# Performance work log

Measured on AMD Instinct MI355X. Metric: run time of the kernel, lower is better.

## Reference

```python
import jax, jax.numpy as jnp
import numpy as np

N = 8192
H = 512
TAU = 0.8
LAM = 0.5
EPS = 1e-8


def setup_inputs() -> dict:
    key = jax.random.key(0)
    k1, k2, k3, k4, k5 = jax.random.split(key, 5)
    xavier_std = 1.414 * np.sqrt(2.0 / (H + H))  # xavier_normal_ with gain=1.414
    return {
        "z_mp": jax.random.normal(k1, (N, H), dtype=jnp.float32),
        "z_sc": jax.random.normal(k2, (N, H), dtype=jnp.float32),
        "pos": jax.random.randint(k3, (N, N), 0, 2, dtype=jnp.int32),
        "W1": (jax.random.normal(k4, (H, H), dtype=jnp.float32) * xavier_std),
        "b1": jnp.zeros((H,), dtype=jnp.float32),
        "W2": (jax.random.normal(k5, (H, H), dtype=jnp.float32) * xavier_std),
        "b2": jnp.zeros((H,), dtype=jnp.float32),
    }


def _proj(z, W1, b1, W2, b2):
    # nn.Linear applies x @ W.T + b
    h = jax.nn.elu(z @ W1.T + b1)
    return h @ W2.T + b2


def _sim(z1, z2, tau):
    # exp(cosine_similarity / tau), computed as in the original:
    # dot(z1, z2.T) / (|z1| |z2|.T) / tau
    n1 = jnp.linalg.norm(z1, axis=-1, keepdims=True)  # [N,1]
    n2 = jnp.linalg.norm(z2, axis=-1, keepdims=True)  # [N,1]
    dot = z1 @ z2.T                                   # [N,N]
    return jnp.exp(dot / (n1 * n2.T) / tau)


def reference(z_mp, z_sc, pos, W1, b1, W2, b2):
    pos_f = pos.astype(jnp.float32)
    zp_mp = _proj(z_mp, W1, b1, W2, b2)
    zp_sc = _proj(z_sc, W1, b1, W2, b2)

    m_mp2sc = _sim(zp_mp, zp_sc, TAU)   # [N,N]
    m_sc2mp = m_mp2sc.T                 # [N,N]

    # row-normalize, masked log-mean (mp -> sc)
    s_mp = m_mp2sc / (jnp.sum(m_mp2sc, axis=1, keepdims=True) + EPS)
    lori_mp = -jnp.mean(jnp.log(jnp.sum(s_mp * pos_f, axis=-1)))

    # row-normalize, masked log-mean (sc -> mp)
    s_sc = m_sc2mp / (jnp.sum(m_sc2mp, axis=1, keepdims=True) + EPS)
    lori_sc = -jnp.mean(jnp.log(jnp.sum(s_sc * pos_f, axis=-1)))

    return LAM * lori_mp + (1.0 - LAM) * lori_sc
```

## Files before the change

### kernel.cpp

```cpp
#include <hip/hip_runtime.h>
#include <stdint.h>


#define NN 8192
#define HH 512
#define TAUF 0.8f
#define EPSF 1e-8f
#define NW (NN / 32)

typedef __attribute__((ext_vector_type(4))) float f32x4;
typedef __attribute__((ext_vector_type(2))) int i32x2;
typedef __attribute__((ext_vector_type(4))) int i32x4;
typedef __attribute__((ext_vector_type(8))) int i32x8;
typedef unsigned short u16;
typedef unsigned int u32;
typedef uint8_t u8;

typedef __attribute__((address_space(1))) void GV;
typedef __attribute__((address_space(3))) void LV;

__device__ __forceinline__ void g2l16(const void* g, void* l) {
  __builtin_amdgcn_global_load_lds((const GV*)g, (LV*)l, 16, 0, 0);
}

__device__ __forceinline__ u32 f2fp8(float x) {
  u32 u = __builtin_bit_cast(u32, x);
  u32 s = (u >> 31) << 7;
  float a = fabsf(x);
  if (a >= 0.015625f) {
    u32 b = __builtin_bit_cast(u32, a);
    b += 0x7FFFFu + ((b >> 20) & 1u);
    u32 e = (b >> 23) - 127u + 7u;
    u32 m = (b >> 20) & 7u;
    return s | (e << 3) | m;
  } else {
    int m = (int)rintf(a * 512.0f);
    return s | (u32)m;
  }
}

__device__ __forceinline__ void cast8f8(const float* __restrict__ in, u8* __restrict__ out, int i) {
  f32x4 a = *(const f32x4*)(in + i);
  f32x4 b = *(const f32x4*)(in + i + 4);
  i32x2 v;
  v.x = (int)(f2fp8(a.x) | (f2fp8(a.y) << 8) | (f2fp8(a.z) << 16) | (f2fp8(a.w) << 24));
  v.y = (int)(f2fp8(b.x) | (f2fp8(b.y) << 8) | (f2fp8(b.z) << 16) | (f2fp8(b.w) << 24));
  *(i32x2*)(out + i) = v;
}

__global__ __launch_bounds__(256)
void prep_kernel(const int* __restrict__ pos, u32* __restrict__ P,
                 const float* __restrict__ z_mp, u8* __restrict__ zbA,
                 const float* __restrict__ z_sc, u8* __restrict__ zbB,
                 const float* __restrict__ W1, u8* __restrict__ W1b,
                 const float* __restrict__ W2, u8* __restrict__ W2b) {
  int b = blockIdx.x, tid = threadIdx.x;
  if (b < 8192) {
    int gid = b * 256 + tid;
    const int* src = pos + (size_t)gid * 32;
    u32 w = 0;
#pragma unroll
    for (int c = 0; c < 8; ++c) {
      i32x4 p = *(const i32x4*)(src + c * 4);
      w |= ((u32)p.x & 1u) << (c * 4);
      w |= ((u32)p.y & 1u) << (c * 4 + 1);
      w |= ((u32)p.z & 1u) << (c * 4 + 2);
      w |= ((u32)p.w & 1u) << (c * 4 + 3);
    }
    P[gid] = w;
  } else if (b < 10240) {
    cast8f8(z_mp, zbA, ((b - 8192) * 256 + tid) * 8);
  } else if (b < 12288) {
    cast8f8(z_sc, zbB, ((b - 10240) * 256 + tid) * 8);
  } else if (b < 12416) {
    cast8f8(W1, W1b, ((b - 12288) * 256 + tid) * 8);
  } else {
    cast8f8(W2, W2b, ((b - 12416) * 256 + tid) * 8);
  }
}

__global__ __launch_bounds__(256, 1)
void proj_fused(const u8* __restrict__ zbA, const u8* __restrict__ zbB,
                const u8* __restrict__ W1b, const float* __restrict__ b1,
                const u8* __restrict__ W2b, const float* __restrict__ b2,
                u8* __restrict__ znA, u8* __restrict__ znB) {
  __shared__ __align__(16) u8 Az[64 * 512];
  __shared__ __align__(16) u8 Hs[64 * 512];
  __shared__ __align__(16) u8 Ws[512 * 128];
  __shared__ float ssqL[4][64];
  __shared__ float invL[64];

  const int tid = threadIdx.x;
  const int lane = tid & 63, w = tid >> 6;
  const int lo = lane & 15, quad = lane >> 4;
  const int b = blockIdx.x;
  const bool isA = b < 128;
  const int m0 = (b & 127) * 64;
  const u8* zb = isA ? zbA : zbB;
  u8* zn = isA ? znA : znB;
  const float nscale = isA ? (1.0f / TAUF) : 1.0f;

  char* AzB = (char*)Az;
  char* HsB = (char*)Hs;
  char* WsB = (char*)Ws;

  {
    const int ls = lane >> 5;
    const int ch = lane & 31;
#pragma unroll
    for (int t = 0; t < 8; ++t) {
      int r = w * 16 + t * 2 + ls;
      int sw = (t * 2 + ls) & 7;
      const u8* src = zb + (size_t)(m0 + r) * HH + ((ch & ~7) | ((ch & 7) ^ sw)) * 16;
      g2l16(src, AzB + w * 8192 + t * 1024);
    }
  }
  const int srow = lane >> 3;
  const int schunk = ((lane & 7) ^ srow) * 16;
  auto stageW = [&](const u8* __restrict__ Wb, int kbyte) {
#pragma unroll
    for (int t = 0; t < 16; ++t)
      g2l16(Wb + (size_t)(w * 128 + t * 8 + srow) * HH + kbyte + schunk,
            WsB + w * 16384 + t * 1024);
  };
  stageW(W1b, 0);
  asm volatile("s_waitcnt vmcnt(0)" ::: "memory");
  __syncthreads();

  f32x4 acc[4][8];

#pragma unroll
  for (int mi = 0; mi < 4; ++mi)
#pragma unroll
    for (int ni = 0; ni < 8; ++ni) acc[mi][ni] = f32x4{0.f, 0.f, 0.f, 0.f};

#pragma unroll
  for (int k0 = 0; k0 < 4; ++k0) {
    i32x8 aF[4], bF[8];
#pragma unroll
    for (int mi = 0; mi < 4; ++mi) {
      int ar = mi * 16 + lo, sw = lo & 7;
      i32x4 p0 = *(const i32x4*)(AzB + ar * 512 + k0 * 128 + ((2 * quad) ^ sw) * 16);
      i32x4 p1 = *(const i32x4*)(AzB + ar * 512 + k0 * 128 + ((2 * quad + 1) ^ sw) * 16);
      aF[mi] = __builtin_shufflevector(p0, p1, 0, 1, 2, 3, 4, 5, 6, 7);
    }
#pragma unroll
    for (int ni = 0; ni < 8; ++ni) {
      int br = w * 128 + ni * 16 + lo, sw = br & 7;
      i32x4 p0 = *(const i32x4*)(WsB + br * 128 + ((2 * quad) ^ sw) * 16);
      i32x4 p1 = *(const i32x4*)(WsB + br * 128 + ((2 * quad + 1) ^ sw) * 16);
      bF[ni] = __builtin_shufflevector(p0, p1, 0, 1, 2, 3, 4, 5, 6, 7);
    }
    __syncthreads();
    if (k0 < 3) stageW(W1b, (k0 + 1) * 128);
    else        stageW(W2b, 0);
#pragma unroll
    for (int mi = 0; mi < 4; ++mi)
#pragma unroll
      for (int ni = 0; ni < 8; ++ni)
        acc[mi][ni] = __builtin_amdgcn_mfma_scale_f32_16x16x128_f8f6f4(
            aF[mi], bF[ni], acc[mi][ni], 0, 0, 0, 127, 0, 127);
    if (k0 < 3) __syncthreads();
  }

  {
    float b1v[8];
#pragma unroll
    for (int ni = 0; ni < 8; ++ni) b1v[ni] = b1[w * 128 + ni * 16 + lo];
#pragma unroll
    for (int mi = 0; mi < 4; ++mi)
#pragma unroll
      for (int r = 0; r < 4; ++r) {
        int row = mi * 16 + quad * 4 + r;
        int rsw = row & 7;
#pragma unroll
        for (int ni = 0; ni < 8; ++ni) {
          float v = acc[mi][ni][r] + b1v[ni];
          if (v < 0.f) v = __expf(v) - 1.f;
          int ch = w * 8 + ni;
          HsB[row * 512 + (((ch & 7) ^ rsw) | (ch & ~7)) * 16 + lo] = (char)(u8)f2fp8(v);
        }
      }
  }
  __syncthreads();

#pragma unroll
  for (int mi = 0; mi < 4; ++mi)
#pragma unroll
    for (int ni = 0; ni < 8; ++ni) acc[mi][ni] = f32x4{0.f, 0.f, 0.f, 0.f};

#pragma unroll
  for (int k0 = 0; k0 < 4; ++k0) {
    i32x8 aF[4], bF[8];
#pragma unroll
    for (int mi = 0; mi < 4; ++mi) {
      int ar = mi * 16 + lo, sw = lo & 7;
      i32x4 p0 = *(const i32x4*)(HsB + ar * 512 + k0 * 128 + ((2 * quad) ^ sw) * 16);
      i32x4 p1 = *(const i32x4*)(HsB + ar * 512 + k0 * 128 + ((2 * quad + 1) ^ sw) * 16);
      aF[mi] = __builtin_shufflevector(p0, p1, 0, 1, 2, 3, 4, 5, 6, 7);
    }
#pragma unroll
    for (int ni = 0; ni < 8; ++ni) {
      int br = w * 128 + ni * 16 + lo, sw = br & 7;
      i32x4 p0 = *(const i32x4*)(WsB + br * 128 + ((2 * quad) ^ sw) * 16);
      i32x4 p1 = *(const i32x4*)(WsB + br * 128 + ((2 * quad + 1) ^ sw) * 16);
      bF[ni] = __builtin_shufflevector(p0, p1, 0, 1, 2, 3, 4, 5, 6, 7);
    }
    if (k0 < 3) {
      __syncthreads();
      stageW(W2b, (k0 + 1) * 128);
    }
#pragma unroll
    for (int mi = 0; mi < 4; ++mi)
#pragma unroll
      for (int ni = 0; ni < 8; ++ni)
        acc[mi][ni] = __builtin_amdgcn_mfma_scale_f32_16x16x128_f8f6f4(
            aF[mi], bF[ni], acc[mi][ni], 0, 0, 0, 127, 0, 127);
    if (k0 < 3) __syncthreads();
  }

  float ssq[4][4] = {};
  {
    float b2v[8];
#pragma unroll
    for (int ni = 0; ni < 8; ++ni) b2v[ni] = b2[w * 128 + ni * 16 + lo];
#pragma unroll
    for (int mi = 0; mi < 4; ++mi)
#pragma unroll
      for (int ni = 0; ni < 8; ++ni)
#pragma unroll
        for (int r = 0; r < 4; ++r) {
          float v = acc[mi][ni][r] + b2v[ni];
          acc[mi][ni][r] = v;
          ssq[mi][r] += v * v;
        }
  }
#pragma unroll
  for (int d = 1; d < 16; d <<= 1)
#pragma unroll
    for (int mi = 0; mi < 4; ++mi)
#pragma unroll
      for (int r = 0; r < 4; ++r) ssq[mi][r] += __shfl_xor(ssq[mi][r], d, 64);
  if (lo == 0) {
#pragma unroll
    for (int mi = 0; mi < 4; ++mi)
#pragma unroll
      for (int r = 0; r < 4; ++r) ssqL[w][mi * 16 + quad * 4 + r] = ssq[mi][r];
  }
  __syncthreads();
  if (tid < 64)
    invL[tid] = nscale * rsqrtf(ssqL[0][tid] + ssqL[1][tid] + ssqL[2][tid] + ssqL[3][tid]);
  __syncthreads();

#pragma unroll
  for (int mi = 0; mi < 4; ++mi)
#pragma unroll
    for (int r = 0; r < 4; ++r) {
      int row = mi * 16 + quad * 4 + r;
      float inv = invL[row];
#pragma unroll
      for (int ni = 0; ni < 8; ++ni)
        AzB[row * 512 + w * 128 + ni * 16 + lo] = (char)(u8)f2fp8(acc[mi][ni][r] * inv);
    }
  __syncthreads();
  {
    int row = tid >> 2, seg = tid & 3;
#pragma unroll
    for (int i = 0; i < 8; ++i) {
      i32x4 v = *(const i32x4*)(AzB + row * 512 + seg * 128 + i * 16);
      *(i32x4*)(zn + (size_t)(m0 + row) * 512 + seg * 128 + i * 16) = v;
    }
  }
}

__global__ __launch_bounds__(256)
void sim_kernel(const u8* __restrict__ Az, const u8* __restrict__ Bz,
                const u32* __restrict__ Pbits,
                float* __restrict__ rowpart, float* __restrict__ posrowpart,
                float* __restrict__ colpart, float* __restrict__ poscolpart) {
  __shared__ __align__(16) u8 As[128 * 128];
  __shared__ __align__(16) u8 Bs[128 * 128];
  __shared__ u32 PBi[128 * 4];
  __shared__ u32 PBj[128 * 4];
  const int tid = threadIdx.x;
  const int lane = tid & 63, w = tid >> 6;
  const int lo = lane & 15, quad = lane >> 4;
  const int wy = w >> 1, wx = w & 1;

  const int bid = blockIdx.x + (int)gridDim.x * blockIdx.y;
  const int xcd = bid & 7, s = bid >> 3;
  const int by = xcd * 8 + (s >> 6);
  const int bx = s & 63;
  const int i0 = by * 128, j0 = bx * 128;

  const int il = tid >> 1, w2 = (tid & 1) * 2;
  const u32* PiSrc = Pbits + (size_t)(i0 + il) * NW + (j0 >> 5) + w2;
  const u32* PjSrc = Pbits + (size_t)(j0 + il) * NW + (i0 >> 5) + w2;
  u32 pa0 = PiSrc[0], pa1 = PiSrc[1], pb0 = PjSrc[0], pb1 = PjSrc[1];

  const int srow = lane >> 3;
  const int schunk = ((lane & 7) ^ srow) * 16;
  char* AsB = (char*)As; char* BsB = (char*)Bs;
  f32x4 acc[4][4] = {};

  for (int k0 = 0; k0 < HH; k0 += 128) {
    const u8* ga = Az + (size_t)(i0 + w * 32 + srow) * HH + k0 + schunk;
    const u8* gb = Bz + (size_t)(j0 + w * 32 + srow) * HH + k0 + schunk;
#pragma unroll
    for (int t = 0; t < 4; ++t) {
      g2l16(ga + (size_t)(t * 8) * HH, AsB + w * 4096 + t * 1024);
      g2l16(gb + (size_t)(t * 8) * HH, BsB + w * 4096 + t * 1024);
    }
    asm volatile("s_waitcnt vmcnt(0)" ::: "memory");
    __syncthreads();
    i32x8 aF[4], bF[4];
#pragma unroll
    for (int mi = 0; mi < 4; ++mi) {
      int ar = wy * 64 + mi * 16 + lo;
      int sw = ar & 7;
      i32x4 p0 = *(const i32x4*)(AsB + ar * 128 + ((2 * quad) ^ sw) * 16);
      i32x4 p1 = *(const i32x4*)(AsB + ar * 128 + ((2 * quad + 1) ^ sw) * 16);
      aF[mi] = __builtin_shufflevector(p0, p1, 0, 1, 2, 3, 4, 5, 6, 7);
    }
#pragma unroll
    for (int ni = 0; ni < 4; ++ni) {
      int br = wx * 64 + ni * 16 + lo;
      int sw = br & 7;
      i32x4 p0 = *(const i32x4*)(BsB + br * 128 + ((2 * quad) ^ sw) * 16);
      i32x4 p1 = *(const i32x4*)(BsB + br * 128 + ((2 * quad + 1) ^ sw) * 16);
      bF[ni] = __builtin_shufflevector(p0, p1, 0, 1, 2, 3, 4, 5, 6, 7);
    }
#pragma unroll
    for (int mi = 0; mi < 4; ++mi)
#pragma unroll
      for (int ni = 0; ni < 4; ++ni)
        acc[mi][ni] = __builtin_amdgcn_mfma_scale_f32_16x16x128_f8f6f4(
            aF[mi], bF[ni], acc[mi][ni], 0, 0, 0, 127, 0, 127);
    __syncthreads();
  }

  PBi[il * 4 + w2] = pa0; PBi[il * 4 + w2 + 1] = pa1;
  PBj[il * 4 + w2] = pb0; PBj[il * 4 + w2 + 1] = pb1;

#pragma unroll
  for (int mi = 0; mi < 4; ++mi)
#pragma unroll
    for (int ni = 0; ni < 4; ++ni)
#pragma unroll
      for (int r = 0; r < 4; ++r)
        acc[mi][ni][r] = __expf(acc[mi][ni][r]);

  __syncthreads();

  const int rowb = wy * 64 + quad * 4;
  const int colb = wx * 64 + lo;

#pragma unroll
  for (int mi = 0; mi < 4; ++mi) {
    int rl = rowb + mi * 16;
    float rs[4], pr[4];
#pragma unroll
    for (int r = 0; r < 4; ++r) {
      u32 W0 = PBi[(rl + r) * 4 + wx * 2];
      u32 W1 = PBi[(rl + r) * 4 + wx * 2 + 1];
      float e0 = acc[mi][0][r], e1 = acc[mi][1][r];
      float e2 = acc[mi][2][r], e3 = acc[mi][3][r];
      rs[r] = (e0 + e1) + (e2 + e3);
      pr[r] = (((W0 >> lo) & 1u) ? e0 : 0.f) + (((W0 >> (16 + lo)) & 1u) ? e1 : 0.f) +
              (((W1 >> lo) & 1u) ? e2 : 0.f) + (((W1 >> (16 + lo)) & 1u) ? e3 : 0.f);
    }
#pragma unroll
    for (int d = 1; d < 16; d <<= 1) {
#pragma unroll
      for (int r = 0; r < 4; ++r) {
        rs[r] += __shfl_xor(rs[r], d, 64);
        pr[r] += __shfl_xor(pr[r], d, 64);
      }
    }
    if (lo == 0) {
      float* rp = rowpart + (size_t)(bx * 2 + wx) * NN;
      float* pp = posrowpart + (size_t)(bx * 2 + wx) * NN;
#pragma unroll
      for (int r = 0; r < 4; ++r) {
        rp[i0 + rl + r] = rs[r];
        pp[i0 + rl + r] = pr[r];
      }
    }
  }

#pragma unroll
  for (int ni = 0; ni < 4; ++ni) {
    int cl = colb + ni * 16;
    u32 W0 = PBj[cl * 4 + wy * 2];
    u32 W1 = PBj[cl * 4 + wy * 2 + 1];
    float cs = 0.f, pc = 0.f;
#pragma unroll
    for (int mi = 0; mi < 4; ++mi) {
      u32 W = (mi < 2) ? W0 : W1;
      int sh = (mi & 1) * 16 + quad * 4;
#pragma unroll
      for (int r = 0; r < 4; ++r) {
        float e = acc[mi][ni][r];
        cs += e;
        pc += ((W >> (sh + r)) & 1u) ? e : 0.f;
      }
    }
    cs += __shfl_xor(cs, 16, 64); cs += __shfl_xor(cs, 32, 64);
    pc += __shfl_xor(pc, 16, 64); pc += __shfl_xor(pc, 32, 64);
    if (quad == 0) {
      colpart[(size_t)(by * 2 + wy) * NN + j0 + cl] = cs;
      poscolpart[(size_t)(by * 2 + wy) * NN + j0 + cl] = pc;
    }
  }
}

__global__ __launch_bounds__(256)
void reduce1_kernel(const float* __restrict__ rowpart, const float* __restrict__ posrowpart,
                    const float* __restrict__ colpart, const float* __restrict__ poscolpart,
                    float* __restrict__ red) {
  int t = threadIdx.x;
  int i = blockIdx.x * 128 + (t >> 1);
  int half = t & 1;
  float rs = 0.f, pr = 0.f, cs = 0.f, pc = 0.f;
  for (int s = half * 64; s < half * 64 + 64; ++s) {
    rs += rowpart[(size_t)s * NN + i];
    pr += posrowpart[(size_t)s * NN + i];
    cs += colpart[(size_t)s * NN + i];
    pc += poscolpart[(size_t)s * NN + i];
  }
  rs += __shfl_xor(rs, 1, 64); pr += __shfl_xor(pr, 1, 64);
  cs += __shfl_xor(cs, 1, 64); pc += __shfl_xor(pc, 1, 64);
  float term = (half == 0) ? (__logf(pr / (rs + EPSF)) + __logf(pc / (cs + EPSF))) : 0.f;
#pragma unroll
  for (int d = 2; d < 64; d <<= 1) term += __shfl_xor(term, d, 64);
  __shared__ float rsh[4];
  if ((t & 63) == 0) rsh[t >> 6] = term;
  __syncthreads();
  if (t == 0) red[blockIdx.x] = rsh[0] + rsh[1] + rsh[2] + rsh[3];
}

__global__ void reduce2_kernel(const float* __restrict__ red, float* __restrict__ out) {
  float s = red[threadIdx.x];
#pragma unroll
  for (int d = 1; d < 64; d <<= 1) s += __shfl_xor(s, d, 64);
  if (threadIdx.x == 0) out[0] = -0.5f * s / (float)NN;
}

extern "C" void kernel_launch(void* const* d_in, const int* in_sizes, int n_in,
                              void* d_out, int out_size, void* d_ws, size_t ws_size,
                              hipStream_t stream) {
  const float* z_mp = (const float*)d_in[0];
  const float* z_sc = (const float*)d_in[1];
  const int* pos = (const int*)d_in[2];
  const float* W1 = (const float*)d_in[3];
  const float* b1 = (const float*)d_in[4];
  const float* W2 = (const float*)d_in[5];
  const float* b2 = (const float*)d_in[6];
  float* out = (float*)d_out;

  char* ws = (char*)d_ws;
  u32* Pbits = (u32*)(ws);
  u8* zbA = (u8*)(ws + 8388608);
  u8* zbB = (u8*)(ws + 16777216);
  u8* W1b = (u8*)(ws + 25165824);
  u8* W2b = (u8*)(ws + 25690112);
  float* rowpart    = (float*)(ws + 26214400);
  float* posrowpart = (float*)(ws + 30408704);
  float* colpart    = (float*)(ws + 34603008);
  float* poscolpart = (float*)(ws + 38797312);
  float* red64 = (float*)(ws + 76546048);

  prep_kernel<<<12544, 256, 0, stream>>>(pos, Pbits, z_mp, zbA, z_sc, zbB, W1, W1b, W2, W2b);

  proj_fused<<<256, 256, 0, stream>>>(zbA, zbB, W1b, b1, W2b, b2, zbA, zbB);

  dim3 gs(64, 64);
  sim_kernel<<<gs, 256, 0, stream>>>(zbA, zbB, Pbits, rowpart, posrowpart, colpart, poscolpart);
  reduce1_kernel<<<64, 256, 0, stream>>>(rowpart, posrowpart, colpart, poscolpart, red64);
  reduce2_kernel<<<1, 64, 0, stream>>>(red64, out);
}
```

Before: 523.8 us.

## Fold pos bit-packing and z fp8 cast into projection kernel, overlapping with MFMA

Pos bit-packing and the z-to-fp8 cast move out of the separate prep kernel into the projection kernel. The pos loads are interleaved between MFMA batches so the 256 MB pos read overlaps the projection matmuls. The projection block is widened to 512 threads (8 waves, 64 output columns each), which halves per-wave accumulators. The aim is to hide the pos bandwidth cost behind compute and drop a launch, at the risk of only 256 blocks limiting memory parallelism for the pos stream.

```diff
diff --git a/kernel.cpp b/kernel.cpp
--- a/kernel.cpp
+++ b/kernel.cpp
@@ -39,55 +39,37 @@
   }
 }
 
+__device__ __forceinline__ u32 pack4f8(f32x4 f) {
+  return f2fp8(f.x) | (f2fp8(f.y) << 8) | (f2fp8(f.z) << 16) | (f2fp8(f.w) << 24);
+}
+
 __device__ __forceinline__ void cast8f8(const float* __restrict__ in, u8* __restrict__ out, int i) {
   f32x4 a = *(const f32x4*)(in + i);
   f32x4 b = *(const f32x4*)(in + i + 4);
   i32x2 v;
-  v.x = (int)(f2fp8(a.x) | (f2fp8(a.y) << 8) | (f2fp8(a.z) << 16) | (f2fp8(a.w) << 24));
-  v.y = (int)(f2fp8(b.x) | (f2fp8(b.y) << 8) | (f2fp8(b.z) << 16) | (f2fp8(b.w) << 24));
+  v.x = (int)pack4f8(a);
+  v.y = (int)pack4f8(b);
   *(i32x2*)(out + i) = v;
 }
 
 __global__ __launch_bounds__(256)
-void prep_kernel(const int* __restrict__ pos, u32* __restrict__ P,
-                 const float* __restrict__ z_mp, u8* __restrict__ zbA,
-                 const float* __restrict__ z_sc, u8* __restrict__ zbB,
-                 const float* __restrict__ W1, u8* __restrict__ W1b,
-                 const float* __restrict__ W2, u8* __restrict__ W2b) {
+void prep_w(const float* __restrict__ W1, u8* __restrict__ W1b,
+            const float* __restrict__ W2, u8* __restrict__ W2b) {
   int b = blockIdx.x, tid = threadIdx.x;
-  if (b < 8192) {
-    int gid = b * 256 + tid;
-    const int* src = pos + (size_t)gid * 32;
-    u32 w = 0;
-#pragma unroll
-    for (int c = 0; c < 8; ++c) {
-      i32x4 p = *(const i32x4*)(src + c * 4);
-      w |= ((u32)p.x & 1u) << (c * 4);
-      w |= ((u32)p.y & 1u) << (c * 4 + 1);
-      w |= ((u32)p.z & 1u) << (c * 4 + 2);
-      w |= ((u32)p.w & 1u) << (c * 4 + 3);
-    }
-    P[gid] = w;
-  } else if (b < 10240) {
-    cast8f8(z_mp, zbA, ((b - 8192) * 256 + tid) * 8);
-  } else if (b < 12288) {
-    cast8f8(z_sc, zbB, ((b - 10240) * 256 + tid) * 8);
-  } else if (b < 12416) {
-    cast8f8(W1, W1b, ((b - 12288) * 256 + tid) * 8);
-  } else {
-    cast8f8(W2, W2b, ((b - 12416) * 256 + tid) * 8);
-  }
-}
-
-__global__ __launch_bounds__(256, 1)
-void proj_fused(const u8* __restrict__ zbA, const u8* __restrict__ zbB,
+  if (b < 128) cast8f8(W1, W1b, (b * 256 + tid) * 8);
+  else         cast8f8(W2, W2b, ((b - 128) * 256 + tid) * 8);
+}
+
+__global__ __launch_bounds__(512, 2)
+void proj_fused(const float* __restrict__ zA, const float* __restrict__ zB,
                 const u8* __restrict__ W1b, const float* __restrict__ b1,
                 const u8* __restrict__ W2b, const float* __restrict__ b2,
-                u8* __restrict__ znA, u8* __restrict__ znB) {
+                u8* __restrict__ znA, u8* __restrict__ znB,
+                const int* __restrict__ pos, u32* __restrict__ Pbits) {
   __shared__ __align__(16) u8 Az[64 * 512];
   __shared__ __align__(16) u8 Hs[64 * 512];
   __shared__ __align__(16) u8 Ws[512 * 128];
-  __shared__ float ssqL[4][64];
+  __shared__ float ssqL[8][64];
   __shared__ float invL[64];
 
   const int tid = threadIdx.x;
@@ -96,7 +78,7 @@
   const int b = blockIdx.x;
   const bool isA = b < 128;
   const int m0 = (b & 127) * 64;
-  const u8* zb = isA ? zbA : zbB;
+  const float* zsrcM = isA ? zA : zB;
   u8* zn = isA ? znA : znB;
   const float nscale = isA ? (1.0f / TAUF) : 1.0f;
 
@@ -104,39 +86,64 @@
   char* HsB = (char*)Hs;
   char* WsB = (char*)Ws;
 
-  {
-    const int ls = lane >> 5;
-    const int ch = lane & 31;
-#pragma unroll
-    for (int t = 0; t < 8; ++t) {
-      int r = w * 16 + t * 2 + ls;
-      int sw = (t * 2 + ls) & 7;
-      const u8* src = zb + (size_t)(m0 + r) * HH + ((ch & ~7) | ((ch & 7) ^ sw)) * 16;
-      g2l16(src, AzB + w * 8192 + t * 1024);
-    }
-  }
   const int srow = lane >> 3;
   const int schunk = ((lane & 7) ^ srow) * 16;
   auto stageW = [&](const u8* __restrict__ Wb, int kbyte) {
 #pragma unroll
-    for (int t = 0; t < 16; ++t)
-      g2l16(Wb + (size_t)(w * 128 + t * 8 + srow) * HH + kbyte + schunk,
-            WsB + w * 16384 + t * 1024);
+    for (int t = 0; t < 8; ++t)
+      g2l16(Wb + (size_t)(w * 64 + t * 8 + srow) * HH + kbyte + schunk,
+            WsB + w * 8192 + t * 1024);
   };
+
+  const size_t posbase = (size_t)b * 32 * NN;
+  auto posIssue = [&](int sp, i32x4* pv) {
+    const i32x4* src = (const i32x4*)(pos + posbase + (size_t)(sp * 512 + tid) * 32);
+#pragma unroll
+    for (int c = 0; c < 8; ++c) pv[c] = src[c];
+  };
+  auto posPack = [&](int sp, const i32x4* pv) {
+    u32 wv = 0;
+#pragma unroll
+    for (int c = 0; c < 8; ++c) {
+      wv |= ((u32)pv[c].x & 1u) << (c * 4);
+      wv |= ((u32)pv[c].y & 1u) << (c * 4 + 1);
+      wv |= ((u32)pv[c].z & 1u) << (c * 4 + 2);
+      wv |= ((u32)pv[c].w & 1u) << (c * 4 + 3);
+    }
+    Pbits[(size_t)b * 8192 + sp * 512 + tid] = wv;
+  };
+
   stageW(W1b, 0);
-  asm volatile("s_waitcnt vmcnt(0)" ::: "memory");
-  __syncthreads();
-
-  f32x4 acc[4][8];
+  {
+    const int r = tid >> 3;
+    const int cb = tid & 7;
+    const float* zsrc = zsrcM + (size_t)(m0 + r) * HH;
+    const int rsw = r & 7;
+#pragma unroll
+    for (int t = 0; t < 4; ++t) {
+      int ch = cb + t * 8;
+      f32x4 f0 = *(const f32x4*)(zsrc + ch * 16 + 0);
+      f32x4 f1 = *(const f32x4*)(zsrc + ch * 16 + 4);
+      f32x4 f2 = *(const f32x4*)(zsrc + ch * 16 + 8);
+      f32x4 f3 = *(const f32x4*)(zsrc + ch * 16 + 12);
+      i32x4 o;
+      o.x = (int)pack4f8(f0); o.y = (int)pack4f8(f1);
+      o.z = (int)pack4f8(f2); o.w = (int)pack4f8(f3);
+      *(i32x4*)(AzB + r * 512 + (((ch & 7) ^ rsw) | (ch & ~7)) * 16) = o;
+    }
+  }
+  __syncthreads();
+
+  f32x4 acc[4][4];
 
 #pragma unroll
   for (int mi = 0; mi < 4; ++mi)
 #pragma unroll
-    for (int ni = 0; ni < 8; ++ni) acc[mi][ni] = f32x4{0.f, 0.f, 0.f, 0.f};
+    for (int ni = 0; ni < 4; ++ni) acc[mi][ni] = f32x4{0.f, 0.f, 0.f, 0.f};
 
 #pragma unroll
   for (int k0 = 0; k0 < 4; ++k0) {
-    i32x8 aF[4], bF[8];
+    i32x8 aF[4], bF[4];
 #pragma unroll
     for (int mi = 0; mi < 4; ++mi) {
       int ar = mi * 16 + lo, sw = lo & 7;
@@ -145,8 +152,8 @@
       aF[mi] = __builtin_shufflevector(p0, p1, 0, 1, 2, 3, 4, 5, 6, 7);
     }
 #pragma unroll
-    for (int ni = 0; ni < 8; ++ni) {
-      int br = w * 128 + ni * 16 + lo, sw = br & 7;
+    for (int ni = 0; ni < 4; ++ni) {
+      int br = w * 64 + ni * 16 + lo, sw = lo & 7;
       i32x4 p0 = *(const i32x4*)(WsB + br * 128 + ((2 * quad) ^ sw) * 16);
       i32x4 p1 = *(const i32x4*)(WsB + br * 128 + ((2 * quad + 1) ^ sw) * 16);
       bF[ni] = __builtin_shufflevector(p0, p1, 0, 1, 2, 3, 4, 5, 6, 7);
@@ -154,19 +161,32 @@
     __syncthreads();
     if (k0 < 3) stageW(W1b, (k0 + 1) * 128);
     else        stageW(W2b, 0);
-#pragma unroll
-    for (int mi = 0; mi < 4; ++mi)
-#pragma unroll
-      for (int ni = 0; ni < 8; ++ni)
-        acc[mi][ni] = __builtin_amdgcn_mfma_scale_f32_16x16x128_f8f6f4(
-            aF[mi], bF[ni], acc[mi][ni], 0, 0, 0, 127, 0, 127);
+    {
+      i32x4 pv[8];
+      posIssue(2 * k0, pv);
+#pragma unroll
+      for (int mi = 0; mi < 4; ++mi)
+#pragma unroll
+        for (int ni = 0; ni < 2; ++ni)
+          acc[mi][ni] = __builtin_amdgcn_mfma_scale_f32_16x16x128_f8f6f4(
+              aF[mi], bF[ni], acc[mi][ni], 0, 0, 0, 127, 0, 127);
+      posPack(2 * k0, pv);
+      posIssue(2 * k0 + 1, pv);
+#pragma unroll
+      for (int mi = 0; mi < 4; ++mi)
+#pragma unroll
+        for (int ni = 2; ni < 4; ++ni)
+          acc[mi][ni] = __builtin_amdgcn_mfma_scale_f32_16x16x128_f8f6f4(
+              aF[mi], bF[ni], acc[mi][ni], 0, 0, 0, 127, 0, 127);
+      posPack(2 * k0 + 1, pv);
+    }
     if (k0 < 3) __syncthreads();
   }
 
   {
-    float b1v[8];
-#pragma unroll
-    for (int ni = 0; ni < 8; ++ni) b1v[ni] = b1[w * 128 + ni * 16 + lo];
+    float b1v[4];
+#pragma unroll
+    for (int ni = 0; ni < 4; ++ni) b1v[ni] = b1[w * 64 + ni * 16 + lo];
 #pragma unroll
     for (int mi = 0; mi < 4; ++mi)
 #pragma unroll
@@ -174,10 +194,10 @@
         int row = mi * 16 + quad * 4 + r;
         int rsw = row & 7;
 #pragma unroll
-        for (int ni = 0; ni < 8; ++ni) {
+        for (int ni = 0; ni < 4; ++ni) {
           float v = acc[mi][ni][r] + b1v[ni];
           if (v < 0.f) v = __expf(v) - 1.f;
-          int ch = w * 8 + ni;
+          int ch = w * 4 + ni;
           HsB[row * 512 + (((ch & 7) ^ rsw) | (ch & ~7)) * 16 + lo] = (char)(u8)f2fp8(v);
         }
       }
@@ -187,11 +207,11 @@
 #pragma unroll
   for (int mi = 0; mi < 4; ++mi)
 #pragma unroll
-    for (int ni = 0; ni < 8; ++ni) acc[mi][ni] = f32x4{0.f, 0.f, 0.f, 0.f};
+    for (int ni = 0; ni < 4; ++ni) acc[mi][ni] = f32x4{0.f, 0.f, 0.f, 0.f};
 
 #pragma unroll
   for (int k0 = 0; k0 < 4; ++k0) {
-    i32x8 aF[4], bF[8];
+    i32x8 aF[4], bF[4];
 #pragma unroll
     for (int mi = 0; mi < 4; ++mi) {
       int ar = mi * 16 + lo, sw = lo & 7;
@@ -200,8 +220,8 @@
       aF[mi] = __builtin_shufflevector(p0, p1, 0, 1, 2, 3, 4, 5, 6, 7);
     }
 #pragma unroll
-    for (int ni = 0; ni < 8; ++ni) {
-      int br = w * 128 + ni * 16 + lo, sw = br & 7;
+    for (int ni = 0; ni < 4; ++ni) {
+      int br = w * 64 + ni * 16 + lo, sw = lo & 7;
       i32x4 p0 = *(const i32x4*)(WsB + br * 128 + ((2 * quad) ^ sw) * 16);
       i32x4 p1 = *(const i32x4*)(WsB + br * 128 + ((2 * quad + 1) ^ sw) * 16);
       bF[ni] = __builtin_shufflevector(p0, p1, 0, 1, 2, 3, 4, 5, 6, 7);
@@ -210,24 +230,37 @@
       __syncthreads();
       stageW(W2b, (k0 + 1) * 128);
     }
-#pragma unroll
-    for (int mi = 0; mi < 4; ++mi)
-#pragma unroll
-      for (int ni = 0; ni < 8; ++ni)
-        acc[mi][ni] = __builtin_amdgcn_mfma_scale_f32_16x16x128_f8f6f4(
-            aF[mi], bF[ni], acc[mi][ni], 0, 0, 0, 127, 0, 127);
+    {
+      i32x4 pv[8];
+      posIssue(8 + 2 * k0, pv);
+#pragma unroll
+      for (int mi = 0; mi < 4; ++mi)
+#pragma unroll
+        for (int ni = 0; ni < 2; ++ni)
+          acc[mi][ni] = __builtin_amdgcn_mfma_scale_f32_16x16x128_f8f6f4(
+              aF[mi], bF[ni], acc[mi][ni], 0, 0, 0, 127, 0, 127);
+      posPack(8 + 2 * k0, pv);
+      posIssue(9 + 2 * k0, pv);
+#pragma unroll
+      for (int mi = 0; mi < 4; ++mi)
+#pragma unroll
+        for (int ni = 2; ni < 4; ++ni)
+          acc[mi][ni] = __builtin_amdgcn_mfma_scale_f32_16x16x128_f8f6f4(
+              aF[mi], bF[ni], acc[mi][ni], 0, 0, 0, 127, 0, 127);
+      posPack(9 + 2 * k0, pv);
+    }
     if (k0 < 3) __syncthreads();
   }
 
   float ssq[4][4] = {};
   {
-    float b2v[8];
-#pragma unroll
-    for (int ni = 0; ni < 8; ++ni) b2v[ni] = b2[w * 128 + ni * 16 + lo];
+    float b2v[4];
+#pragma unroll
+    for (int ni = 0; ni < 4; ++ni) b2v[ni] = b2[w * 64 + ni * 16 + lo];
 #pragma unroll
     for (int mi = 0; mi < 4; ++mi)
 #pragma unroll
-      for (int ni = 0; ni < 8; ++ni)
+      for (int ni = 0; ni < 4; ++ni)
 #pragma unroll
         for (int r = 0; r < 4; ++r) {
           float v = acc[mi][ni][r] + b2v[ni];
@@ -248,8 +281,11 @@
       for (int r = 0; r < 4; ++r) ssqL[w][mi * 16 + quad * 4 + r] = ssq[mi][r];
   }
   __syncthreads();
-  if (tid < 64)
-    invL[tid] = nscale * rsqrtf(ssqL[0][tid] + ssqL[1][tid] + ssqL[2][tid] + ssqL[3][tid]);
+  if (tid < 64) {
+    float s = ssqL[0][tid] + ssqL[1][tid] + ssqL[2][tid] + ssqL[3][tid] +
+              ssqL[4][tid] + ssqL[5][tid] + ssqL[6][tid] + ssqL[7][tid];
+    invL[tid] = nscale * rsqrtf(s);
+  }
   __syncthreads();
 
 #pragma unroll
@@ -259,16 +295,16 @@
       int row = mi * 16 + quad * 4 + r;
       float inv = invL[row];
 #pragma unroll
-      for (int ni = 0; ni < 8; ++ni)
-        AzB[row * 512 + w * 128 + ni * 16 + lo] = (char)(u8)f2fp8(acc[mi][ni][r] * inv);
+      for (int ni = 0; ni < 4; ++ni)
+        AzB[row * 512 + w * 64 + ni * 16 + lo] = (char)(u8)f2fp8(acc[mi][ni][r] * inv);
     }
   __syncthreads();
   {
-    int row = tid >> 2, seg = tid & 3;
-#pragma unroll
-    for (int i = 0; i < 8; ++i) {
-      i32x4 v = *(const i32x4*)(AzB + row * 512 + seg * 128 + i * 16);
-      *(i32x4*)(zn + (size_t)(m0 + row) * 512 + seg * 128 + i * 16) = v;
+    int row = tid >> 3, seg = tid & 7;
+#pragma unroll
+    for (int i = 0; i < 4; ++i) {
+      i32x4 v = *(const i32x4*)(AzB + row * 512 + seg * 64 + i * 16);
+      *(i32x4*)(zn + (size_t)(m0 + row) * 512 + seg * 64 + i * 16) = v;
     }
   }
 }
@@ -470,9 +506,9 @@
   float* poscolpart = (float*)(ws + 38797312);
   float* red64 = (float*)(ws + 76546048);
 
-  prep_kernel<<<12544, 256, 0, stream>>>(pos, Pbits, z_mp, zbA, z_sc, zbB, W1, W1b, W2, W2b);
-
-  proj_fused<<<256, 256, 0, stream>>>(zbA, zbB, W1b, b1, W2b, b2, zbA, zbB);
+  prep_w<<<256, 256, 0, stream>>>(W1, W1b, W2, W2b);
+
+  proj_fused<<<256, 512, 0, stream>>>(z_mp, z_sc, W1b, b1, W2b, b2, zbA, zbB, pos, Pbits);
 
   dim3 gs(64, 64);
   sim_kernel<<<gs, 256, 0, stream>>>(zbA, zbB, Pbits, rowpart, posrowpart, colpart, poscolpart);
```

Result: no change. 533.5 us (+1.9%).

## Double-buffer sim kernel LDS tiles and fold final reduction into reduce1 via atomics

Applied to the files above, without the earlier changes.

The similarity GEMM now keeps two LDS buffers for the A and B fp8 tiles. The next K-slice is issued with global_load_lds before the MFMAs on the current slice, so memory fetch can overlap compute, and the last barrier is dropped. The second reduction kernel is removed: reduce1 blocks atomically add their partial sums and use a counter so the last block writes the output. The accumulator and counter are zeroed in prep_kernel. This doubles the LDS per block, which may lower occupancy. It also relies on the barrier waiting for the asynchronous LDS loads, since the explicit vmcnt wait is gone.

```diff
diff --git a/kernel.cpp b/kernel.cpp
--- a/kernel.cpp
+++ b/kernel.cpp
@@ -53,8 +53,13 @@
                  const float* __restrict__ z_mp, u8* __restrict__ zbA,
                  const float* __restrict__ z_sc, u8* __restrict__ zbB,
                  const float* __restrict__ W1, u8* __restrict__ W1b,
-                 const float* __restrict__ W2, u8* __restrict__ W2b) {
+                 const float* __restrict__ W2, u8* __restrict__ W2b,
+                 float* __restrict__ red) {
   int b = blockIdx.x, tid = threadIdx.x;
+  if (b == 0 && tid == 0) {
+    red[0] = 0.f;
+    ((u32*)red)[1] = 0u;
+  }
   if (b < 8192) {
     int gid = b * 256 + tid;
     const int* src = pos + (size_t)gid * 32;
@@ -278,8 +283,8 @@
                 const u32* __restrict__ Pbits,
                 float* __restrict__ rowpart, float* __restrict__ posrowpart,
                 float* __restrict__ colpart, float* __restrict__ poscolpart) {
-  __shared__ __align__(16) u8 As[128 * 128];
-  __shared__ __align__(16) u8 Bs[128 * 128];
+  __shared__ __align__(16) u8 As[2 * 128 * 128];
+  __shared__ __align__(16) u8 Bs[2 * 128 * 128];
   __shared__ u32 PBi[128 * 4];
   __shared__ u32 PBj[128 * 4];
   const int tid = threadIdx.x;
@@ -303,31 +308,38 @@
   char* AsB = (char*)As; char* BsB = (char*)Bs;
   f32x4 acc[4][4] = {};
 
-  for (int k0 = 0; k0 < HH; k0 += 128) {
-    const u8* ga = Az + (size_t)(i0 + w * 32 + srow) * HH + k0 + schunk;
-    const u8* gb = Bz + (size_t)(j0 + w * 32 + srow) * HH + k0 + schunk;
+  auto stage = [&](int buf, int kbyte) {
+    const u8* ga = Az + (size_t)(i0 + w * 32 + srow) * HH + kbyte + schunk;
+    const u8* gb = Bz + (size_t)(j0 + w * 32 + srow) * HH + kbyte + schunk;
 #pragma unroll
     for (int t = 0; t < 4; ++t) {
-      g2l16(ga + (size_t)(t * 8) * HH, AsB + w * 4096 + t * 1024);
-      g2l16(gb + (size_t)(t * 8) * HH, BsB + w * 4096 + t * 1024);
-    }
-    asm volatile("s_waitcnt vmcnt(0)" ::: "memory");
-    __syncthreads();
+      g2l16(ga + (size_t)(t * 8) * HH, AsB + buf * 16384 + w * 4096 + t * 1024);
+      g2l16(gb + (size_t)(t * 8) * HH, BsB + buf * 16384 + w * 4096 + t * 1024);
+    }
+  };
+
+  stage(0, 0);
+  __syncthreads();
+
+#pragma unroll
+  for (int t = 0; t < 4; ++t) {
+    const int cur = t & 1;
+    if (t < 3) stage(cur ^ 1, (t + 1) * 128);
     i32x8 aF[4], bF[4];
 #pragma unroll
     for (int mi = 0; mi < 4; ++mi) {
       int ar = wy * 64 + mi * 16 + lo;
       int sw = ar & 7;
-      i32x4 p0 = *(const i32x4*)(AsB + ar * 128 + ((2 * quad) ^ sw) * 16);
-      i32x4 p1 = *(const i32x4*)(AsB + ar * 128 + ((2 * quad + 1) ^ sw) * 16);
+      i32x4 p0 = *(const i32x4*)(AsB + cur * 16384 + ar * 128 + ((2 * quad) ^ sw) * 16);
+      i32x4 p1 = *(const i32x4*)(AsB + cur * 16384 + ar * 128 + ((2 * quad + 1) ^ sw) * 16);
       aF[mi] = __builtin_shufflevector(p0, p1, 0, 1, 2, 3, 4, 5, 6, 7);
     }
 #pragma unroll
     for (int ni = 0; ni < 4; ++ni) {
       int br = wx * 64 + ni * 16 + lo;
       int sw = br & 7;
-      i32x4 p0 = *(const i32x4*)(BsB + br * 128 + ((2 * quad) ^ sw) * 16);
-      i32x4 p1 = *(const i32x4*)(BsB + br * 128 + ((2 * quad + 1) ^ sw) * 16);
+      i32x4 p0 = *(const i32x4*)(BsB + cur * 16384 + br * 128 + ((2 * quad) ^ sw) * 16);
+      i32x4 p1 = *(const i32x4*)(BsB + cur * 16384 + br * 128 + ((2 * quad + 1) ^ sw) * 16);
       bF[ni] = __builtin_shufflevector(p0, p1, 0, 1, 2, 3, 4, 5, 6, 7);
     }
 #pragma unroll
@@ -336,7 +348,7 @@
       for (int ni = 0; ni < 4; ++ni)
         acc[mi][ni] = __builtin_amdgcn_mfma_scale_f32_16x16x128_f8f6f4(
             aF[mi], bF[ni], acc[mi][ni], 0, 0, 0, 127, 0, 127);
-    __syncthreads();
+    if (t < 3) __syncthreads();
   }
 
   PBi[il * 4 + w2] = pa0; PBi[il * 4 + w2 + 1] = pa1;
@@ -417,7 +429,7 @@
 __global__ __launch_bounds__(256)
 void reduce1_kernel(const float* __restrict__ rowpart, const float* __restrict__ posrowpart,
                     const float* __restrict__ colpart, const float* __restrict__ poscolpart,
-                    float* __restrict__ red) {
+                    float* __restrict__ red, float* __restrict__ out) {
   int t = threadIdx.x;
   int i = blockIdx.x * 128 + (t >> 1);
   int half = t & 1;
@@ -436,14 +448,16 @@
   __shared__ float rsh[4];
   if ((t & 63) == 0) rsh[t >> 6] = term;
   __syncthreads();
-  if (t == 0) red[blockIdx.x] = rsh[0] + rsh[1] + rsh[2] + rsh[3];
-}
-
-__global__ void reduce2_kernel(const float* __restrict__ red, float* __restrict__ out) {
-  float s = red[threadIdx.x];
-#pragma unroll
-  for (int d = 1; d < 64; d <<= 1) s += __shfl_xor(s, d, 64);
-  if (threadIdx.x == 0) out[0] = -0.5f * s / (float)NN;
+  if (t == 0) {
+    float bs = rsh[0] + rsh[1] + rsh[2] + rsh[3];
+    atomicAdd(&red[0], bs);
+    __threadfence();
+    u32 old = atomicAdd((u32*)red + 1, 1u);
+    if (old == 63u) {
+      float total = atomicAdd(&red[0], 0.0f);
+      out[0] = -0.5f * total / (float)NN;
+    }
+  }
 }
 
 extern "C" void kernel_launch(void* const* d_in, const int* in_sizes, int n_in,
@@ -470,12 +484,12 @@
   float* poscolpart = (float*)(ws + 38797312);
   float* red64 = (float*)(ws + 76546048);
 
-  prep_kernel<<<12544, 256, 0, stream>>>(pos, Pbits, z_mp, zbA, z_sc, zbB, W1, W1b, W2, W2b);
+  prep_kernel<<<12544, 256, 0, stream>>>(pos, Pbits, z_mp, zbA, z_sc, zbB, W1, W1b, W2, W2b,
+                                         red64);
 
   proj_fused<<<256, 256, 0, stream>>>(zbA, zbB, W1b, b1, W2b, b2, zbA, zbB);
 
   dim3 gs(64, 64);
   sim_kernel<<<gs, 256, 0, stream>>>(zbA, zbB, Pbits, rowpart, posrowpart, colpart, poscolpart);
-  reduce1_kernel<<<64, 256, 0, stream>>>(rowpart, posrowpart, colpart, poscolpart, red64);
-  reduce2_kernel<<<1, 64, 0, stream>>>(red64, out);
-}
+  reduce1_kernel<<<64, 256, 0, stream>>>(rowpart, posrowpart, colpart, poscolpart, red64, out);
+}
```

Result: no change. 527.5 us (+0.7%).

## Fuse z fp8 cast into projection and reduce sums via atomics in sim kernel

Applied to the files above, without the earlier changes.

The fp32-to-fp8 cast of z_mp and z_sc moves out of the prep kernel and into the projection kernel, which now reads fp32 rows and writes swizzled fp8 into shared memory itself. The sim kernel no longer writes per-block partial row and column sums for separate reduce kernels. It accumulates them with global atomicAdd, and the last block, found through an atomic counter, computes the final loss. This removes two kernel launches, the large partial-sum buffers, and an intermediate fp8 round trip through global memory. In exchange it adds atomic contention, float summation order that is no longer deterministic, and a serial final reduction run by a single block.

```diff
diff --git a/kernel.cpp b/kernel.cpp
--- a/kernel.cpp
+++ b/kernel.cpp
@@ -39,22 +39,28 @@
   }
 }
 
+__device__ __forceinline__ u32 pack4f8(f32x4 f) {
+  return f2fp8(f.x) | (f2fp8(f.y) << 8) | (f2fp8(f.z) << 16) | (f2fp8(f.w) << 24);
+}
+
 __device__ __forceinline__ void cast8f8(const float* __restrict__ in, u8* __restrict__ out, int i) {
   f32x4 a = *(const f32x4*)(in + i);
   f32x4 b = *(const f32x4*)(in + i + 4);
   i32x2 v;
-  v.x = (int)(f2fp8(a.x) | (f2fp8(a.y) << 8) | (f2fp8(a.z) << 16) | (f2fp8(a.w) << 24));
-  v.y = (int)(f2fp8(b.x) | (f2fp8(b.y) << 8) | (f2fp8(b.z) << 16) | (f2fp8(b.w) << 24));
+  v.x = (int)pack4f8(a);
+  v.y = (int)pack4f8(b);
   *(i32x2*)(out + i) = v;
 }
 
 __global__ __launch_bounds__(256)
 void prep_kernel(const int* __restrict__ pos, u32* __restrict__ P,
-                 const float* __restrict__ z_mp, u8* __restrict__ zbA,
-                 const float* __restrict__ z_sc, u8* __restrict__ zbB,
                  const float* __restrict__ W1, u8* __restrict__ W1b,
-                 const float* __restrict__ W2, u8* __restrict__ W2b) {
+                 const float* __restrict__ W2, u8* __restrict__ W2b,
+                 float* __restrict__ rowsum, float* __restrict__ posrow,
+                 float* __restrict__ colsum, float* __restrict__ poscol,
+                 u32* __restrict__ cnt) {
   int b = blockIdx.x, tid = threadIdx.x;
+  if (b == 0 && tid == 0) cnt[0] = 0u;
   if (b < 8192) {
     int gid = b * 256 + tid;
     const int* src = pos + (size_t)gid * 32;
@@ -68,19 +74,18 @@
       w |= ((u32)p.w & 1u) << (c * 4 + 3);
     }
     P[gid] = w;
-  } else if (b < 10240) {
-    cast8f8(z_mp, zbA, ((b - 8192) * 256 + tid) * 8);
-  } else if (b < 12288) {
-    cast8f8(z_sc, zbB, ((b - 10240) * 256 + tid) * 8);
-  } else if (b < 12416) {
-    cast8f8(W1, W1b, ((b - 12288) * 256 + tid) * 8);
+  } else if (b < 8320) {
+    cast8f8(W1, W1b, ((b - 8192) * 256 + tid) * 8);
+  } else if (b < 8448) {
+    cast8f8(W2, W2b, ((b - 8320) * 256 + tid) * 8);
   } else {
-    cast8f8(W2, W2b, ((b - 12416) * 256 + tid) * 8);
+    int gid = (b - 8448) * 256 + tid;
+    rowsum[gid] = 0.f; posrow[gid] = 0.f; colsum[gid] = 0.f; poscol[gid] = 0.f;
   }
 }
 
 __global__ __launch_bounds__(256, 1)
-void proj_fused(const u8* __restrict__ zbA, const u8* __restrict__ zbB,
+void proj_fused(const float* __restrict__ zA, const float* __restrict__ zB,
                 const u8* __restrict__ W1b, const float* __restrict__ b1,
                 const u8* __restrict__ W2b, const float* __restrict__ b2,
                 u8* __restrict__ znA, u8* __restrict__ znB) {
@@ -96,7 +101,7 @@
   const int b = blockIdx.x;
   const bool isA = b < 128;
   const int m0 = (b & 127) * 64;
-  const u8* zb = isA ? zbA : zbB;
+  const float* zsrcM = isA ? zA : zB;
   u8* zn = isA ? znA : znB;
   const float nscale = isA ? (1.0f / TAUF) : 1.0f;
 
@@ -104,17 +109,6 @@
   char* HsB = (char*)Hs;
   char* WsB = (char*)Ws;
 
-  {
-    const int ls = lane >> 5;
-    const int ch = lane & 31;
-#pragma unroll
-    for (int t = 0; t < 8; ++t) {
-      int r = w * 16 + t * 2 + ls;
-      int sw = (t * 2 + ls) & 7;
-      const u8* src = zb + (size_t)(m0 + r) * HH + ((ch & ~7) | ((ch & 7) ^ sw)) * 16;
-      g2l16(src, AzB + w * 8192 + t * 1024);
-    }
-  }
   const int srow = lane >> 3;
   const int schunk = ((lane & 7) ^ srow) * 16;
   auto stageW = [&](const u8* __restrict__ Wb, int kbyte) {
@@ -123,7 +117,26 @@
       g2l16(Wb + (size_t)(w * 128 + t * 8 + srow) * HH + kbyte + schunk,
             WsB + w * 16384 + t * 1024);
   };
+
   stageW(W1b, 0);
+  {
+    const int row = tid >> 2;
+    const int q = tid & 3;
+    const float* zsrc = zsrcM + (size_t)(m0 + row) * HH + q * 128;
+    const int rsw = row & 7;
+#pragma unroll
+    for (int c = 0; c < 8; ++c) {
+      int ch = q * 8 + c;
+      f32x4 f0 = *(const f32x4*)(zsrc + c * 16);
+      f32x4 f1 = *(const f32x4*)(zsrc + c * 16 + 4);
+      f32x4 f2 = *(const f32x4*)(zsrc + c * 16 + 8);
+      f32x4 f3 = *(const f32x4*)(zsrc + c * 16 + 12);
+      i32x4 o;
+      o.x = (int)pack4f8(f0); o.y = (int)pack4f8(f1);
+      o.z = (int)pack4f8(f2); o.w = (int)pack4f8(f3);
+      *(i32x4*)(AzB + row * 512 + (((ch & 7) ^ rsw) | (ch & ~7)) * 16) = o;
+    }
+  }
   asm volatile("s_waitcnt vmcnt(0)" ::: "memory");
   __syncthreads();
 
@@ -276,12 +289,15 @@
 __global__ __launch_bounds__(256)
 void sim_kernel(const u8* __restrict__ Az, const u8* __restrict__ Bz,
                 const u32* __restrict__ Pbits,
-                float* __restrict__ rowpart, float* __restrict__ posrowpart,
-                float* __restrict__ colpart, float* __restrict__ poscolpart) {
+                float* __restrict__ rowsum, float* __restrict__ posrow,
+                float* __restrict__ colsum, float* __restrict__ poscol,
+                u32* __restrict__ cnt, float* __restrict__ out) {
   __shared__ __align__(16) u8 As[128 * 128];
   __shared__ __align__(16) u8 Bs[128 * 128];
   __shared__ u32 PBi[128 * 4];
   __shared__ u32 PBj[128 * 4];
+  __shared__ int lastFlag;
+  __shared__ float rsh[4];
   const int tid = threadIdx.x;
   const int lane = tid & 63, w = tid >> 6;
   const int lo = lane & 15, quad = lane >> 4;
@@ -378,12 +394,10 @@
       }
     }
     if (lo == 0) {
-      float* rp = rowpart + (size_t)(bx * 2 + wx) * NN;
-      float* pp = posrowpart + (size_t)(bx * 2 + wx) * NN;
 #pragma unroll
       for (int r = 0; r < 4; ++r) {
-        rp[i0 + rl + r] = rs[r];
-        pp[i0 + rl + r] = pr[r];
+        atomicAdd(&rowsum[i0 + rl + r], rs[r]);
+        atomicAdd(&posrow[i0 + rl + r], pr[r]);
       }
     }
   }
@@ -408,42 +422,33 @@
     cs += __shfl_xor(cs, 16, 64); cs += __shfl_xor(cs, 32, 64);
     pc += __shfl_xor(pc, 16, 64); pc += __shfl_xor(pc, 32, 64);
     if (quad == 0) {
-      colpart[(size_t)(by * 2 + wy) * NN + j0 + cl] = cs;
-      poscolpart[(size_t)(by * 2 + wy) * NN + j0 + cl] = pc;
-    }
-  }
-}
-
-__global__ __launch_bounds__(256)
-void reduce1_kernel(const float* __restrict__ rowpart, const float* __restrict__ posrowpart,
-                    const float* __restrict__ colpart, const float* __restrict__ poscolpart,
-                    float* __restrict__ red) {
-  int t = threadIdx.x;
-  int i = blockIdx.x * 128 + (t >> 1);
-  int half = t & 1;
-  float rs = 0.f, pr = 0.f, cs = 0.f, pc = 0.f;
-  for (int s = half * 64; s < half * 64 + 64; ++s) {
-    rs += rowpart[(size_t)s * NN + i];
-    pr += posrowpart[(size_t)s * NN + i];
-    cs += colpart[(size_t)s * NN + i];
-    pc += poscolpart[(size_t)s * NN + i];
-  }
-  rs += __shfl_xor(rs, 1, 64); pr += __shfl_xor(pr, 1, 64);
-  cs += __shfl_xor(cs, 1, 64); pc += __shfl_xor(pc, 1, 64);
-  float term = (half == 0) ? (__logf(pr / (rs + EPSF)) + __logf(pc / (cs + EPSF))) : 0.f;
-#pragma unroll
-  for (int d = 2; d < 64; d <<= 1) term += __shfl_xor(term, d, 64);
-  __shared__ float rsh[4];
-  if ((t & 63) == 0) rsh[t >> 6] = term;
-  __syncthreads();
-  if (t == 0) red[blockIdx.x] = rsh[0] + rsh[1] + rsh[2] + rsh[3];
-}
-
-__global__ void reduce2_kernel(const float* __restrict__ red, float* __restrict__ out) {
-  float s = red[threadIdx.x];
-#pragma unroll
-  for (int d = 1; d < 64; d <<= 1) s += __shfl_xor(s, d, 64);
-  if (threadIdx.x == 0) out[0] = -0.5f * s / (float)NN;
+      atomicAdd(&colsum[j0 + cl], cs);
+      atomicAdd(&poscol[j0 + cl], pc);
+    }
+  }
+
+  __syncthreads();
+  if (tid == 0) {
+    __threadfence();
+    u32 old = atomicAdd(cnt, 1u);
+    lastFlag = (old == 4095u) ? 1 : 0;
+  }
+  __syncthreads();
+  if (lastFlag) {
+    float term = 0.f;
+    for (int i = tid; i < NN; i += 256) {
+      float rs = __hip_atomic_load(&rowsum[i], __ATOMIC_RELAXED, __HIP_MEMORY_SCOPE_AGENT);
+      float pr = __hip_atomic_load(&posrow[i], __ATOMIC_RELAXED, __HIP_MEMORY_SCOPE_AGENT);
+      float cs = __hip_atomic_load(&colsum[i], __ATOMIC_RELAXED, __HIP_MEMORY_SCOPE_AGENT);
+      float pc = __hip_atomic_load(&poscol[i], __ATOMIC_RELAXED, __HIP_MEMORY_SCOPE_AGENT);
+      term += __logf(pr / (rs + EPSF)) + __logf(pc / (cs + EPSF));
+    }
+#pragma unroll
+    for (int d = 1; d < 64; d <<= 1) term += __shfl_xor(term, d, 64);
+    if ((tid & 63) == 0) rsh[tid >> 6] = term;
+    __syncthreads();
+    if (tid == 0) out[0] = -0.5f * (rsh[0] + rsh[1] + rsh[2] + rsh[3]) / (float)NN;
+  }
 }
 
 extern "C" void kernel_launch(void* const* d_in, const int* in_sizes, int n_in,
@@ -460,22 +465,22 @@
 
   char* ws = (char*)d_ws;
   u32* Pbits = (u32*)(ws);
-  u8* zbA = (u8*)(ws + 8388608);
-  u8* zbB = (u8*)(ws + 16777216);
+  u8* znA = (u8*)(ws + 8388608);
+  u8* znB = (u8*)(ws + 16777216);
   u8* W1b = (u8*)(ws + 25165824);
   u8* W2b = (u8*)(ws + 25690112);
-  float* rowpart    = (float*)(ws + 26214400);
-  float* posrowpart = (float*)(ws + 30408704);
-  float* colpart    = (float*)(ws + 34603008);
-  float* poscolpart = (float*)(ws + 38797312);
-  float* red64 = (float*)(ws + 76546048);
-
-  prep_kernel<<<12544, 256, 0, stream>>>(pos, Pbits, z_mp, zbA, z_sc, zbB, W1, W1b, W2, W2b);
-
-  proj_fused<<<256, 256, 0, stream>>>(zbA, zbB, W1b, b1, W2b, b2, zbA, zbB);
+  float* rowsum = (float*)(ws + 26214400);
+  float* posrow = (float*)(ws + 26247168);
+  float* colsum = (float*)(ws + 26279936);
+  float* poscol = (float*)(ws + 26312704);
+  u32* cnt = (u32*)(ws + 76546048);
+
+  prep_kernel<<<8480, 256, 0, stream>>>(pos, Pbits, W1, W1b, W2, W2b,
+                                        rowsum, posrow, colsum, poscol, cnt);
+
+  proj_fused<<<256, 256, 0, stream>>>(z_mp, z_sc, W1b, b1, W2b, b2, znA, znB);
 
   dim3 gs(64, 64);
-  sim_kernel<<<gs, 256, 0, stream>>>(zbA, zbB, Pbits, rowpart, posrowpart, colpart, poscolpart);
-  reduce1_kernel<<<64, 256, 0, stream>>>(rowpart, posrowpart, colpart, poscolpart, red64);
-  reduce2_kernel<<<1, 64, 0, stream>>>(red64, out);
-}
+  sim_kernel<<<gs, 256, 0, stream>>>(znA, znB, Pbits,
+                                     rowsum, posrow, colsum, poscol, cnt, out);
+}
```

Result: slower. 800.9 us (+52.9%).
